# Optimization experiments

Hardware: AMD Instinct MI355X
Metric: run time of the kernel (lower is better)

Reference implementation:

```python
import jax, jax.numpy as jnp
import numpy as np

B, H, W, C = 32, 56, 56, 512
HEADS, WS, SS = 16, 7, 3
N = WS * WS            # window area = 49
HD = C // HEADS        # head dim = 32
HID = 4 * C            # mlp hidden = 2048
nWh, nWw = H // WS, W // WS
nW = nWh * nWw


def _rel_pos_index():
    # static (N, N) int index into relative_position_bias_table
    coords = np.stack(np.meshgrid(np.arange(WS), np.arange(WS), indexing='ij'))  # (2, WS, WS)
    cf = coords.reshape(2, -1)                       # (2, N)
    rel = (cf[:, :, None] - cf[:, None, :]).transpose(1, 2, 0).copy()  # (N, N, 2)
    rel[:, :, 0] += WS - 1
    rel[:, :, 1] += WS - 1
    rel[:, :, 0] *= 2 * WS - 1
    return rel.sum(-1)  # (N, N)


def _attn_mask():
    # static shifted-window attention mask, (nW, N, N) with 0 / -100
    img = np.zeros((H, W))
    cnt = 0
    for h0, h1 in ((0, H - WS), (H - WS, H - SS), (H - SS, H)):
        for w0, w1 in ((0, W - WS), (W - WS, W - SS), (W - SS, W)):
            img[h0:h1, w0:w1] = cnt
            cnt += 1
    mw = img.reshape(nWh, WS, nWw, WS).transpose(0, 2, 1, 3).reshape(-1, N)  # (nW, N)
    diff = mw[:, None, :] - mw[:, :, None]
    return np.where(diff != 0, -100.0, 0.0).astype(np.float32)

_REL_IDX = _rel_pos_index()
_MASK = _attn_mask()


def _ln(x, g, b, eps=1e-5):
    mu = x.mean(-1, keepdims=True)
    var = ((x - mu) ** 2).mean(-1, keepdims=True)
    return (x - mu) * jax.lax.rsqrt(var + eps) * g + b


def setup_inputs() -> dict:
    key = jax.random.key(0)
    ks = jax.random.split(key, 8)
    s = lambda k, shape: jax.random.normal(k, shape, jnp.float32) * 0.02
    return {
        'x': jax.random.normal(ks[0], (B, H, W, C), jnp.float32),
        'norm1_g': jnp.ones((C,), jnp.float32), 'norm1_b': jnp.zeros((C,), jnp.float32),
        'qkv_w': s(ks[1], (3 * C, C)), 'qkv_b': jnp.zeros((3 * C,), jnp.float32),
        'rel_pos_table': s(ks[2], ((2 * WS - 1) ** 2, HEADS)),
        'proj_w': s(ks[3], (C, C)), 'proj_b': jnp.zeros((C,), jnp.float32),
        'norm2_g': jnp.ones((C,), jnp.float32), 'norm2_b': jnp.zeros((C,), jnp.float32),
        'fc1_w': s(ks[4], (HID, C)), 'fc1_b': jnp.zeros((HID,), jnp.float32),
        'fc2_w': s(ks[5], (C, HID)), 'fc2_b': jnp.zeros((C,), jnp.float32),
    }


def reference(x, norm1_g, norm1_b, qkv_w, qkv_b, rel_pos_table, proj_w, proj_b,
              norm2_g, norm2_b, fc1_w, fc1_b, fc2_w, fc2_b):
    shortcut = x
    y = _ln(x, norm1_g, norm1_b)
    # cyclic shift
    y = jnp.roll(y, (-SS, -SS), axis=(1, 2))
    # window partition -> (B*nW, N, C)
    yw = y.reshape(B, nWh, WS, nWw, WS, C).transpose(0, 1, 3, 2, 4, 5).reshape(B * nW, N, C)
    # qkv projection
    qkv = yw @ qkv_w.T + qkv_b
    qkv = qkv.reshape(B * nW, N, 3, HEADS, HD).transpose(2, 0, 3, 1, 4)
    q, k, v = qkv[0], qkv[1], qkv[2]              # each (B*nW, HEADS, N, HD)
    scale = HD ** -0.5
    attn = jnp.einsum('bhqd,bhkd->bhqk', q * scale, k)  # (B*nW, HEADS, N, N)
    # relative position bias gather
    bias = rel_pos_table[jnp.asarray(_REL_IDX.reshape(-1))].reshape(N, N, HEADS)
    attn = attn + bias.transpose(2, 0, 1)[None]
    # shifted-window mask
    attn = attn.reshape(B, nW, HEADS, N, N) + jnp.asarray(_MASK)[None, :, None]
    attn = jax.nn.softmax(attn.reshape(B * nW, HEADS, N, N), axis=-1)
    o = jnp.einsum('bhqk,bhkd->bhqd', attn, v)
    o = o.transpose(0, 2, 1, 3).reshape(B * nW, N, C)
    o = o @ proj_w.T + proj_b
    # window reverse + reverse shift
    o = o.reshape(B, nWh, nWw, WS, WS, C).transpose(0, 1, 3, 2, 4, 5).reshape(B, H, W, C)
    o = jnp.roll(o, (SS, SS), axis=(1, 2))
    x = shortcut + o
    # MLP
    h = _ln(x, norm2_g, norm2_b)
    h = jax.nn.gelu(h @ fc1_w.T + fc1_b, approximate=False)
    h = h @ fc2_w.T + fc2_b
    return x + h
```

## Files before the change

### kernel.cpp

```cpp
#include <hip/hip_runtime.h>

#define Bb   32
#define Hh   56
#define Ww_  56
#define Cc   512
#define HEADS 16
#define WS   7
#define SS   3
#define Nn   49
#define HD   32
#define HID  2048
#define NWIN 2048
#define NTOK 100352

typedef __attribute__((ext_vector_type(4))) float f32x4;
typedef __attribute__((ext_vector_type(8))) short bf16x8;

#define AS1 __attribute__((address_space(1)))
#define AS3 __attribute__((address_space(3)))

__device__ __forceinline__ ushort f2bf(float x) {
  union { float f; unsigned u; } un; un.f = x;
  unsigned u = un.u;
  return (ushort)((u + 0x7fffu + ((u >> 16) & 1u)) >> 16);
}

__global__ void cvtw_kern(const float* __restrict__ s, ushort* __restrict__ d, int n) {
  int i = blockIdx.x * 256 + threadIdx.x;
  if (i < n) d[i] = f2bf(s[i]);
}

__global__ void prep_bias_kern(const float* __restrict__ table, float* __restrict__ be2) {
  int idx = blockIdx.x * 256 + threadIdx.x;
  int h = idx >> 12, q = (idx >> 6) & 63, t = idx & 63;
  int l15 = t >> 2, n = t & 3;
  int key = n * 16 + l15;
  float v = 0.f;
  if (q < Nn && key < Nn) {
    int qi = q / 7, qj = q - qi * 7;
    int ki = key / 7, kj = key - ki * 7;
    v = table[((qi - ki + 6) * 13 + (qj - kj + 6)) * HEADS + h];
  }
  be2[idx] = v;
}

template<int MODE>
__global__ __launch_bounds__(256) void ln_kern(const float* __restrict__ x,
    const float* __restrict__ g, const float* __restrict__ bsh,
    ushort* __restrict__ out)
{
  int row  = blockIdx.x * 4 + (threadIdx.x >> 6);
  int lane = threadIdx.x & 63;
  const float* src;
  if (MODE == 0) {
    unsigned w = (unsigned)row / 49u, n = (unsigned)row - w * 49u;
    unsigned bb = w >> 6, wi = w & 63;
    unsigned wh = wi >> 3, ww = wi & 7;
    unsigned i = n / 7u, j = n - i * 7u;
    unsigned sr = wh * 7 + i + SS; if (sr >= Hh) sr -= Hh;
    unsigned sc = ww * 7 + j + SS; if (sc >= Ww_) sc -= Ww_;
    src = x + ((size_t)(bb * Hh + sr) * Ww_ + sc) * Cc;
  } else {
    src = x + (size_t)row * Cc;
  }
  int c = lane * 8;
  f32x4 v0 = *(const f32x4*)(src + c);
  f32x4 v1 = *(const f32x4*)(src + c + 4);
  float s = 0.f, s2 = 0.f;
  #pragma unroll
  for (int e = 0; e < 4; ++e) { s += v0[e]; s2 += v0[e]*v0[e]; s += v1[e]; s2 += v1[e]*v1[e]; }
  #pragma unroll
  for (int off = 32; off; off >>= 1) { s += __shfl_xor(s, off); s2 += __shfl_xor(s2, off); }
  float mu = s * (1.f / 512.f);
  float rstd = rsqrtf(s2 * (1.f / 512.f) - mu * mu + 1e-5f);
  bf16x8 r;
  #pragma unroll
  for (int e = 0; e < 8; ++e) {
    float xv = (e < 4) ? v0[e] : v1[e - 4];
    r[e] = (short)f2bf((xv - mu) * rstd * g[c + e] + bsh[c + e]);
  }
  *(bf16x8*)(out + (size_t)row * Cc + c) = r;
}

template<int EPI>
__global__ __launch_bounds__(256, 2) void gemm_kern(
    const ushort* __restrict__ A, const ushort* __restrict__ Bw,
    const float* __restrict__ bias, int M, int N, int K,
    void* __restrict__ outp, const float* __restrict__ resid,
    ushort* __restrict__ qb, ushort* __restrict__ kb, ushort* __restrict__ vb)
{
  __shared__ ushort As[128 * 64];
  __shared__ ushort Bs[128 * 64];
  const int tid = threadIdx.x;
  const int wave = tid >> 6, lane = tid & 63;
  const int l15 = lane & 15, lhi = lane >> 4;
  const int sw7 = l15 & 7;

  int gx = gridDim.x;
  int nwg = gx * gridDim.y;
  int orig = blockIdx.y * gx + blockIdx.x;
  int cpx = nwg >> 3;
  int wg = (orig & 7) * cpx + (orig >> 3);
  int bx = wg % gx, by = wg / gx;
  const int brow = by * 128, bcol = bx * 128;

  const int wr = (wave >> 1) * 64, wc = (wave & 1) * 64;

  const int srow = lane >> 3;
  const int schk = ((lane & 7) ^ srow) * 8;
  const ushort* aG = A  + (size_t)(brow + srow) * K + schk;
  const ushort* bG = Bw + (size_t)(bcol + srow) * K + schk;

  f32x4 acc[4][4];
  #pragma unroll
  for (int m = 0; m < 4; ++m)
    #pragma unroll
    for (int n = 0; n < 4; ++n)
      acc[m][n] = (f32x4){0.f, 0.f, 0.f, 0.f};

  for (int k0 = 0; k0 < K; k0 += 64) {
    if (k0) __syncthreads();
    #pragma unroll
    for (int s = 0; s < 4; ++s) {
      int rg = (s * 4 + wave) * 8;
      __builtin_amdgcn_global_load_lds(
        (const AS1 void*)(aG + (size_t)rg * K + k0),
        (AS3 void*)&As[rg * 64], 16, 0, 0);
      __builtin_amdgcn_global_load_lds(
        (const AS1 void*)(bG + (size_t)rg * K + k0),
        (AS3 void*)&Bs[rg * 64], 16, 0, 0);
    }
    __syncthreads();
    #pragma unroll
    for (int kk = 0; kk < 2; ++kk) {
      bf16x8 af[4], bfr[4];
      #pragma unroll
      for (int m = 0; m < 4; ++m) {
        af[m]  = *(const bf16x8*)&As[(wr + m * 16 + l15) * 64 + (((kk * 4 + lhi) ^ sw7)) * 8];
        bfr[m] = *(const bf16x8*)&Bs[(wc + m * 16 + l15) * 64 + (((kk * 4 + lhi) ^ sw7)) * 8];
      }
      #pragma unroll
      for (int m = 0; m < 4; ++m)
        #pragma unroll
        for (int n = 0; n < 4; ++n)
          acc[m][n] = __builtin_amdgcn_mfma_f32_16x16x32_bf16(af[m], bfr[n], acc[m][n], 0, 0, 0);
    }
  }

  float bv[4];
  #pragma unroll
  for (int n = 0; n < 4; ++n) bv[n] = bias[bcol + wc + n * 16 + l15];
  #pragma unroll
  for (int m = 0; m < 4; ++m) {
    int rbase = brow + wr + m * 16 + lhi * 4;
    #pragma unroll
    for (int n = 0; n < 4; ++n) {
      int cc = bcol + wc + n * 16 + l15;
      #pragma unroll
      for (int j = 0; j < 4; ++j) {
        unsigned r = (unsigned)(rbase + j);
        float v = acc[m][n][j] + bv[n];
        if (EPI == 0) {
          unsigned w = r / 49u, nn = r - w * 49u;
          int part = cc >> 9, head = (cc >> 5) & 15, d = cc & 31;
          size_t wh = (size_t)(w * HEADS + head);
          ushort bvs = f2bf(v);
          if (part == 0)      qb[(wh * 64 + nn) * 32 + d] = bvs;
          else if (part == 1) kb[(wh * 64 + nn) * 32 + d] = bvs;
          else                vb[(wh * 32 + d) * 64 + nn] = bvs;
        } else if (EPI == 1) {
          float u2 = v * (1.5957691216f + 0.0713548162f * v * v);
          float gl = __fdividef(v, 1.0f + __expf(-u2));
          ((ushort*)outp)[(size_t)r * N + cc] = f2bf(gl);
        } else if (EPI == 2) {
          unsigned w = r / 49u, nn = r - w * 49u;
          unsigned bb = w >> 6, wi = w & 63;
          unsigned wh = wi >> 3, ww = wi & 7;
          unsigned ii = nn / 7u, jj = nn - ii * 7u;
          unsigned dr = wh * 7 + ii + SS; if (dr >= Hh) dr -= Hh;
          unsigned dc = ww * 7 + jj + SS; if (dc >= Ww_) dc -= Ww_;
          size_t p = ((size_t)bb * Hh + dr) * Ww_ + dc;
          ((float*)outp)[p * Cc + cc] = resid[p * Cc + cc] + v;
        } else {
          float* o = (float*)outp;
          size_t idx = (size_t)r * Cc + cc;
          o[idx] = o[idx] + v;
        }
      }
    }
  }
}

__global__ __launch_bounds__(256) void attn_kern(
    const ushort* __restrict__ qb, const ushort* __restrict__ kb,
    const ushort* __restrict__ vb, const float* __restrict__ be2,
    ushort* __restrict__ o_win)
{
  __shared__ ushort P[4][4096];
  const int wv = threadIdx.x >> 6, lane = threadIdx.x & 63;
  const int l15 = lane & 15, lhi = lane >> 4;
  const int w = blockIdx.x;
  const int head = blockIdx.y * 4 + wv;
  const int wi = w & 63, whh = wi >> 3, www = wi & 7;
  ushort* Pl = P[wv];

  int krg[4];
  #pragma unroll
  for (int n = 0; n < 4; ++n) {
    int key = n * 16 + l15;
    int rg = -1;
    if (key < Nn) {
      int ki = key / 7, kj = key - ki * 7;
      int rr = whh * 7 + ki, cc = www * 7 + kj;
      rg = (rr < 49 ? 0 : (rr < 53 ? 1 : 2)) * 3 + (cc < 49 ? 0 : (cc < 53 ? 1 : 2));
    }
    krg[n] = rg;
  }
  int qrg[4][4];
  #pragma unroll
  for (int m = 0; m < 4; ++m)
    #pragma unroll
    for (int j = 0; j < 4; ++j) {
      int q = m * 16 + lhi * 4 + j;
      int rg = -2;
      if (q < Nn) {
        int qi = q / 7, qj = q - qi * 7;
        int rr = whh * 7 + qi, cc = www * 7 + qj;
        rg = (rr < 49 ? 0 : (rr < 53 ? 1 : 2)) * 3 + (cc < 49 ? 0 : (cc < 53 ? 1 : 2));
      }
      qrg[m][j] = rg;
    }

  const ushort* qp = qb + (size_t)(w * HEADS + head) * 2048;
  const ushort* kp = kb + (size_t)(w * HEADS + head) * 2048;
  const ushort* vp = vb + (size_t)(w * HEADS + head) * 2048;
  const float*  bep = be2 + head * 4096;

  bf16x8 qf[4], kf[4];
  #pragma unroll
  for (int m = 0; m < 4; ++m) {
    qf[m] = *(const bf16x8*)(qp + (m * 16 + l15) * 32 + lhi * 8);
    kf[m] = *(const bf16x8*)(kp + (m * 16 + l15) * 32 + lhi * 8);
  }
  f32x4 sa[4][4];
  #pragma unroll
  for (int m = 0; m < 4; ++m)
    #pragma unroll
    for (int n = 0; n < 4; ++n)
      sa[m][n] = __builtin_amdgcn_mfma_f32_16x16x32_bf16(qf[m], kf[n],
                   (f32x4){0.f, 0.f, 0.f, 0.f}, 0, 0, 0);

  #pragma unroll
  for (int m = 0; m < 4; ++m)
    #pragma unroll
    for (int j = 0; j < 4; ++j) {
      int q = m * 16 + lhi * 4 + j;
      int qr = qrg[m][j];
      f32x4 bev = *(const f32x4*)(bep + q * 64 + l15 * 4);
      float vv[4];
      float mx = -1e30f;
      #pragma unroll
      for (int n = 0; n < 4; ++n) {
        float v;
        if (qr >= 0 && krg[n] >= 0) {
          v = sa[m][n][j] * 0.17677669529663687f + bev[n];
          if (qr != krg[n]) v -= 100.0f;
        } else v = -1e30f;
        vv[n] = v;
        mx = fmaxf(mx, v);
      }
      #pragma unroll
      for (int off = 8; off; off >>= 1) mx = fmaxf(mx, __shfl_xor(mx, off));
      float sum = 0.f;
      #pragma unroll
      for (int n = 0; n < 4; ++n) { float p = __expf(vv[n] - mx); vv[n] = p; sum += p; }
      #pragma unroll
      for (int off = 8; off; off >>= 1) sum += __shfl_xor(sum, off);
      float is = 1.0f / sum;
      #pragma unroll
      for (int n = 0; n < 4; ++n) {
        int bo = (q * 128 + (n * 16 + l15) * 2) ^ ((q & 7) << 4);
        *(ushort*)((char*)Pl + bo) = f2bf(vv[n] * is);
      }
    }

  bf16x8 vf[2][2];
  #pragma unroll
  for (int nt = 0; nt < 2; ++nt)
    #pragma unroll
    for (int kt = 0; kt < 2; ++kt)
      vf[nt][kt] = *(const bf16x8*)(vp + (nt * 16 + l15) * 64 + kt * 32 + lhi * 8);
  f32x4 oa[4][2];
  #pragma unroll
  for (int m = 0; m < 4; ++m)
    #pragma unroll
    for (int nt = 0; nt < 2; ++nt)
      oa[m][nt] = (f32x4){0.f, 0.f, 0.f, 0.f};
  #pragma unroll
  for (int m = 0; m < 4; ++m) {
    int row = m * 16 + l15;
    #pragma unroll
    for (int kt = 0; kt < 2; ++kt) {
      int bo = (row * 128 + kt * 64 + lhi * 16) ^ ((row & 7) << 4);
      bf16x8 pa = *(const bf16x8*)((char*)Pl + bo);
      #pragma unroll
      for (int nt = 0; nt < 2; ++nt)
        oa[m][nt] = __builtin_amdgcn_mfma_f32_16x16x32_bf16(pa, vf[nt][kt], oa[m][nt], 0, 0, 0);
    }
  }
  #pragma unroll
  for (int m = 0; m < 4; ++m) {
    int q0 = m * 16 + lhi * 4;
    #pragma unroll
    for (int nt = 0; nt < 2; ++nt) {
      int d = nt * 16 + l15;
      #pragma unroll
      for (int j = 0; j < 4; ++j) {
        int q = q0 + j;
        if (q < Nn)
          o_win[((size_t)w * Nn + q) * Cc + head * HD + d] = f2bf(oa[m][nt][j]);
      }
    }
  }
}

extern "C" void kernel_launch(void* const* d_in, const int* in_sizes, int n_in,
                              void* d_out, int out_size, void* d_ws, size_t ws_size,
                              hipStream_t stream) {
  const float* x      = (const float*)d_in[0];
  const float* n1g    = (const float*)d_in[1];
  const float* n1b    = (const float*)d_in[2];
  const float* qkv_w  = (const float*)d_in[3];
  const float* qkv_b  = (const float*)d_in[4];
  const float* relt   = (const float*)d_in[5];
  const float* proj_w = (const float*)d_in[6];
  const float* proj_b = (const float*)d_in[7];
  const float* n2g    = (const float*)d_in[8];
  const float* n2b    = (const float*)d_in[9];
  const float* fc1_w  = (const float*)d_in[10];
  const float* fc1_b  = (const float*)d_in[11];
  const float* fc2_w  = (const float*)d_in[12];
  const float* fc2_b  = (const float*)d_in[13];

  char* ws = (char*)d_ws;
  ushort* wq = (ushort*)ws; ws += (size_t)1536 * 512 * 2;
  ushort* wp = (ushort*)ws; ws += (size_t)512 * 512 * 2;
  ushort* w1 = (ushort*)ws; ws += (size_t)2048 * 512 * 2;
  ushort* w2 = (ushort*)ws; ws += (size_t)512 * 2048 * 2;
  float*  be = (float*)ws;  ws += (size_t)16 * 64 * 64 * 4;
  ushort* buf1 = (ushort*)ws; ws += (size_t)NTOK * 2048 * 2;
  ushort* qbuf = (ushort*)ws; ws += (size_t)NWIN * 16 * 64 * 32 * 2;
  ushort* kbuf = (ushort*)ws; ws += (size_t)NWIN * 16 * 64 * 32 * 2;
  ushort* vbuf = (ushort*)ws; ws += (size_t)NWIN * 16 * 64 * 32 * 2;
  ushort* yw = buf1;
  ushort* o_win = buf1;
  ushort* h1 = buf1;
  ushort* l2buf = qbuf;
  float* xout = (float*)d_out;

  cvtw_kern<<<(1536 * 512 + 255) / 256, 256, 0, stream>>>(qkv_w, wq, 1536 * 512);
  cvtw_kern<<<(512 * 512 + 255) / 256, 256, 0, stream>>>(proj_w, wp, 512 * 512);
  cvtw_kern<<<(2048 * 512 + 255) / 256, 256, 0, stream>>>(fc1_w, w1, 2048 * 512);
  cvtw_kern<<<(512 * 2048 + 255) / 256, 256, 0, stream>>>(fc2_w, w2, 512 * 2048);
  prep_bias_kern<<<65536 / 256, 256, 0, stream>>>(relt, be);

  ln_kern<0><<<NTOK / 4, 256, 0, stream>>>(x, n1g, n1b, yw);
  gemm_kern<0><<<dim3(12, 784), 256, 0, stream>>>(yw, wq, qkv_b, NTOK, 1536, 512,
                                                  nullptr, nullptr, qbuf, kbuf, vbuf);
  attn_kern<<<dim3(NWIN, 4), 256, 0, stream>>>(qbuf, kbuf, vbuf, be, o_win);
  gemm_kern<2><<<dim3(4, 784), 256, 0, stream>>>(o_win, wp, proj_b, NTOK, 512, 512,
                                                 xout, x, nullptr, nullptr, nullptr);
  ln_kern<1><<<NTOK / 4, 256, 0, stream>>>(xout, n2g, n2b, l2buf);
  gemm_kern<1><<<dim3(16, 784), 256, 0, stream>>>(l2buf, w1, fc1_b, NTOK, 2048, 512,
                                                  h1, nullptr, nullptr, nullptr, nullptr);
  gemm_kern<3><<<dim3(4, 784), 256, 0, stream>>>(h1, w2, fc2_b, NTOK, 512, 2048,
                                                 xout, xout, nullptr, nullptr, nullptr);
}
```

Measured before the change: 1.341 ms.

## Store Q/K head-major token-contiguous and merge weight conversion launches

Q and K are now written by the QKV GEMM epilogue in a head-major layout indexed by raw token row (padded to NTOKP), dropping the per-element divide by 49 and making each lane's 32-wide writes contiguous along tokens. The attention kernel reads Q/K from offset w*49 in that layout, so window rows are no longer padded to 64 and reads of rows 49-63 spill into the next window (the later mask handles them). The four weight-conversion launches are merged into one grid-stride kernel to cut launch overhead. The buffer shrinks slightly, but stores into Q/K stay scattered across 32-element rows per head.

```diff
diff --git a/kernel.cpp b/kernel.cpp
--- a/kernel.cpp
+++ b/kernel.cpp
@@ -12,6 +12,7 @@
 #define HID  2048
 #define NWIN 2048
 #define NTOK 100352
+#define NTOKP 100416
 
 typedef __attribute__((ext_vector_type(4))) float f32x4;
 typedef __attribute__((ext_vector_type(8))) short bf16x8;
@@ -25,9 +26,16 @@
   return (ushort)((u + 0x7fffu + ((u >> 16) & 1u)) >> 16);
 }
 
-__global__ void cvtw_kern(const float* __restrict__ s, ushort* __restrict__ d, int n) {
+__global__ void cvtw4_kern(const float* __restrict__ s0, ushort* __restrict__ d0, int n0,
+                           const float* __restrict__ s1, ushort* __restrict__ d1, int n1,
+                           const float* __restrict__ s2, ushort* __restrict__ d2, int n2,
+                           const float* __restrict__ s3, ushort* __restrict__ d3, int n3) {
   int i = blockIdx.x * 256 + threadIdx.x;
-  if (i < n) d[i] = f2bf(s[i]);
+  int stride = gridDim.x * 256;
+  for (int k = i; k < n0; k += stride) d0[k] = f2bf(s0[k]);
+  for (int k = i; k < n1; k += stride) d1[k] = f2bf(s1[k]);
+  for (int k = i; k < n2; k += stride) d2[k] = f2bf(s2[k]);
+  for (int k = i; k < n3; k += stride) d3[k] = f2bf(s3[k]);
 }
 
 __global__ void prep_bias_kern(const float* __restrict__ table, float* __restrict__ be2) {
@@ -161,13 +169,14 @@
         unsigned r = (unsigned)(rbase + j);
         float v = acc[m][n][j] + bv[n];
         if (EPI == 0) {
-          unsigned w = r / 49u, nn = r - w * 49u;
           int part = cc >> 9, head = (cc >> 5) & 15, d = cc & 31;
-          size_t wh = (size_t)(w * HEADS + head);
           ushort bvs = f2bf(v);
-          if (part == 0)      qb[(wh * 64 + nn) * 32 + d] = bvs;
-          else if (part == 1) kb[(wh * 64 + nn) * 32 + d] = bvs;
-          else                vb[(wh * 32 + d) * 64 + nn] = bvs;
+          if (part == 0)      qb[((size_t)head * NTOKP + r) * 32 + d] = bvs;
+          else if (part == 1) kb[((size_t)head * NTOKP + r) * 32 + d] = bvs;
+          else {
+            unsigned w = r / 49u, nn = r - w * 49u;
+            vb[(((size_t)(w * HEADS + head)) * 32 + d) * 64 + nn] = bvs;
+          }
         } else if (EPI == 1) {
           float u2 = v * (1.5957691216f + 0.0713548162f * v * v);
           float gl = __fdividef(v, 1.0f + __expf(-u2));
@@ -231,8 +240,8 @@
       qrg[m][j] = rg;
     }
 
-  const ushort* qp = qb + (size_t)(w * HEADS + head) * 2048;
-  const ushort* kp = kb + (size_t)(w * HEADS + head) * 2048;
+  const ushort* qp = qb + ((size_t)head * NTOKP + (size_t)w * 49) * 32;
+  const ushort* kp = kb + ((size_t)head * NTOKP + (size_t)w * 49) * 32;
   const ushort* vp = vb + (size_t)(w * HEADS + head) * 2048;
   const float*  bep = be2 + head * 4096;
 
@@ -349,19 +358,19 @@
   ushort* w2 = (ushort*)ws; ws += (size_t)512 * 2048 * 2;
   float*  be = (float*)ws;  ws += (size_t)16 * 64 * 64 * 4;
   ushort* buf1 = (ushort*)ws; ws += (size_t)NTOK * 2048 * 2;
-  ushort* qbuf = (ushort*)ws; ws += (size_t)NWIN * 16 * 64 * 32 * 2;
-  ushort* kbuf = (ushort*)ws; ws += (size_t)NWIN * 16 * 64 * 32 * 2;
-  ushort* vbuf = (ushort*)ws; ws += (size_t)NWIN * 16 * 64 * 32 * 2;
+  ushort* qbuf = (ushort*)ws; ws += (size_t)16 * NTOKP * 32 * 2;
+  ushort* kbuf = (ushort*)ws; ws += (size_t)16 * NTOKP * 32 * 2;
+  ushort* vbuf = (ushort*)ws; ws += (size_t)NWIN * 16 * 32 * 64 * 2;
   ushort* yw = buf1;
   ushort* o_win = buf1;
   ushort* h1 = buf1;
   ushort* l2buf = qbuf;
   float* xout = (float*)d_out;
 
-  cvtw_kern<<<(1536 * 512 + 255) / 256, 256, 0, stream>>>(qkv_w, wq, 1536 * 512);
-  cvtw_kern<<<(512 * 512 + 255) / 256, 256, 0, stream>>>(proj_w, wp, 512 * 512);
-  cvtw_kern<<<(2048 * 512 + 255) / 256, 256, 0, stream>>>(fc1_w, w1, 2048 * 512);
-  cvtw_kern<<<(512 * 2048 + 255) / 256, 256, 0, stream>>>(fc2_w, w2, 512 * 2048);
+  cvtw4_kern<<<2048, 256, 0, stream>>>(qkv_w, wq, 1536 * 512,
+                                       proj_w, wp, 512 * 512,
+                                       fc1_w, w1, 2048 * 512,
+                                       fc2_w, w2, 512 * 2048);
   prep_bias_kern<<<65536 / 256, 256, 0, stream>>>(relt, be);
 
   ln_kern<0><<<NTOK / 4, 256, 0, stream>>>(x, n1g, n1b, yw);
```

Result: no change. 1.327 ms (-1.1%).
